# Kernel tuning notes

Measured on AMD Instinct MI355X. Metric: run time of the kernel, lower is better.

Reference implementation:

```python
import jax, jax.numpy as jnp
import numpy as np

N = 16384      # nodes per graph (128x128 image)
E = 9 * N      # 8-neighborhood + self edges
C = 512        # input feature channels
M = 32         # matrixSize


def _p(key, shape, scale=0.05):
    return jax.random.normal(key, shape, dtype=jnp.float32) * scale


def setup_inputs() -> dict:
    key = jax.random.key(0)
    ks = jax.random.split(key, 40)
    inp = {
        "cF": jax.random.normal(ks[0], (N, C), dtype=jnp.float32),
        "sF": jax.random.normal(ks[1], (N, C), dtype=jnp.float32),
        "content_edge_index": jax.random.randint(ks[2], (2, E), 0, N),
        "content_selections": jax.random.randint(ks[3], (E,), 0, 9),
        "style_edge_index": jax.random.randint(ks[4], (2, E), 0, N),
        "style_selections": jax.random.randint(ks[5], (E,), 0, 9),
        "compress_W": _p(ks[6], (1, C, M)),   # kernel_size=1 -> 1 selection
        "compress_b": _p(ks[7], (M,)),
        "unzip_W": _p(ks[8], (1, M, C)),
        "unzip_b": _p(ks[9], (C,)),
    }
    i = 10
    for net in ("cnet", "snet"):
        for j, (ci, co) in enumerate([(C, 256), (256, 128), (128, M)], 1):
            inp[f"{net}_W{j}"] = _p(ks[i], (9, ci, co)); i += 1  # kernel_size=3 -> 9 selections
            inp[f"{net}_b{j}"] = _p(ks[i], (co,)); i += 1
        inp[f"{net}_fcW"] = _p(ks[i], (M * M, M * M)); i += 1   # torch Linear [out,in]
        inp[f"{net}_fcb"] = _p(ks[i], (M * M,)); i += 1
    return inp


def sel_conv(x, edge_index, sel, W, b):
    """SelectionConv: per-selection weight, gather from src, scatter-add to dst.
    x: [N,Cin], W: [S,Cin,Cout]. Edges with selection >= S are masked (kernel_size=1)."""
    S = W.shape[0]
    t = jnp.einsum('nc,scd->snd', x, W)              # [S, N, Cout]
    src, dst = edge_index[0], edge_index[1]
    msgs = t[jnp.minimum(sel, S - 1), src]           # [E, Cout]
    msgs = jnp.where((sel < S)[:, None], msgs, 0.0)
    return jax.ops.segment_sum(msgs, dst, num_segments=x.shape[0]) + b


def cnn_net(x, ei, sel, W1, b1, W2, b2, W3, b3, fcW, fcb):
    h = jax.nn.relu(sel_conv(x, ei, sel, W1, b1))
    h = jax.nn.relu(sel_conv(h, ei, sel, W2, b2))
    h = sel_conv(h, ei, sel, W3, b3)                 # [N, M]
    g = (h.T @ h) / h.shape[0]                       # [M, M] gram
    return g.reshape(-1) @ fcW.T + fcb               # [M*M]


def reference(cF, sF, content_edge_index, content_selections, style_edge_index,
              style_selections, compress_W, compress_b, unzip_W, unzip_b,
              cnet_W1, cnet_b1, cnet_W2, cnet_b2, cnet_W3, cnet_b3, cnet_fcW, cnet_fcb,
              snet_W1, snet_b1, snet_W2, snet_b2, snet_W3, snet_b3, snet_fcW, snet_fcb):
    cMean = jnp.mean(cF, axis=0, keepdims=True)
    cFc = cF - cMean
    sMean = jnp.mean(sF, axis=0, keepdims=True)
    sFc = sF - sMean
    compress_content = sel_conv(cFc, content_edge_index, content_selections,
                                compress_W, compress_b)          # [N, M]
    m = compress_W.shape[2]
    cMat = cnn_net(cFc, content_edge_index, content_selections,
                   cnet_W1, cnet_b1, cnet_W2, cnet_b2, cnet_W3, cnet_b3,
                   cnet_fcW, cnet_fcb).reshape(m, m)
    sMat = cnn_net(sFc, style_edge_index, style_selections,
                   snet_W1, snet_b1, snet_W2, snet_b2, snet_W3, snet_b3,
                   snet_fcW, snet_fcb).reshape(m, m)
    transmatrix = sMat @ cMat                                    # [M, M]
    transfeature = (transmatrix @ compress_content.T).T          # [N, M]
    out = sel_conv(transfeature, content_edge_index, content_selections,
                   unzip_W, unzip_b) + sMean                     # [N, 512]
    return (out, transmatrix)
```

## Files before the change

kernel.cpp:

```cpp
#include <hip/hip_runtime.h>
#include <hip/hip_bf16.h>
#include <cstddef>
#include <cstdint>

#define NN 16384
#define EE (9*NN)
#define CC 512

typedef __attribute__((ext_vector_type(4))) float f32x4;
typedef __attribute__((ext_vector_type(8))) short bf16x8;

static inline int idiv(int a, int b){ return (a+b-1)/b; }

__device__ __forceinline__ float bf2f(unsigned short u){
    union{unsigned u; float f;} v; v.u = ((unsigned)u) << 16; return v.f;
}
__device__ __forceinline__ unsigned short f2bf(float f){
    union{float f; unsigned u;} v; v.f = f;
    unsigned r = v.u + 0x7fffu + ((v.u >> 16) & 1u);
    return (unsigned short)(r >> 16);
}

__device__ __forceinline__ void gload16(const void* gsrc, void* ldst){
    __builtin_amdgcn_global_load_lds(
        (const __attribute__((address_space(1))) unsigned int*)gsrc,
        (__attribute__((address_space(3))) unsigned int*)ldst,
        16, 0, 0);
}


__global__ void zero_i(int* __restrict__ p, int n){
    int i = blockIdx.x*256 + threadIdx.x; if (i < n) p[i] = 0;
}

__global__ void colsum2(const float* __restrict__ F0, float* __restrict__ cs0,
                        const float* __restrict__ F1, float* __restrict__ cs1){
    const float* F = blockIdx.z ? F1 : F0;
    float* cs = blockIdx.z ? cs1 : cs0;
    const int RPB = NN/256;
    int r0 = blockIdx.x * RPB;
    int c4 = threadIdx.x;
    float4 s = {0.f,0.f,0.f,0.f};
    for (int r = 0; r < RPB; ++r){
        float4 v = ((const float4*)(F + (size_t)(r0+r)*CC))[c4];
        s.x += v.x; s.y += v.y; s.z += v.z; s.w += v.w;
    }
    atomicAdd(&cs[c4*4+0], s.x);
    atomicAdd(&cs[c4*4+1], s.y);
    atomicAdd(&cs[c4*4+2], s.z);
    atomicAdd(&cs[c4*4+3], s.w);
}

__global__ void center2(const float* __restrict__ F0, const float* __restrict__ cs0,
                        ushort4* __restrict__ o0,
                        const float* __restrict__ F1, const float* __restrict__ cs1,
                        ushort4* __restrict__ o1){
    const float* F = blockIdx.z ? F1 : F0;
    const float* cs = blockIdx.z ? cs1 : cs0;
    ushort4* o = blockIdx.z ? o1 : o0;
    int i = blockIdx.x*256 + threadIdx.x;
    float4 v = ((const float4*)F)[i];
    int c = (i << 2) & (CC-1);
    float4 m = *(const float4*)(cs + c);
    ushort4 r;
    r.x = f2bf(v.x - m.x*(1.f/NN));
    r.y = f2bf(v.y - m.y*(1.f/NN));
    r.z = f2bf(v.z - m.z*(1.f/NN));
    r.w = f2bf(v.w - m.w*(1.f/NN));
    o[i] = r;
}

__global__ void wtransz(const float* __restrict__ W0, unsigned short* __restrict__ Wt0,
                        const float* __restrict__ W1, unsigned short* __restrict__ Wt1,
                        int S, int K, int Cout, int Npad, int Kpad){
    const float* W = blockIdx.z ? W1 : W0;
    unsigned short* Wt = blockIdx.z ? Wt1 : Wt0;
    int idx = blockIdx.x*256 + threadIdx.x;
    if (idx >= Npad*Kpad) return;
    int colp = idx / Kpad, k = idx - colp*Kpad;
    int s = colp / Cout, j = colp - s*Cout;
    float v = 0.f;
    if (s < S && k < K) v = W[((size_t)s*K + k)*Cout + j];
    Wt[idx] = f2bf(v);
}

__global__ void wtrans2z(const float* __restrict__ W0, const float* __restrict__ W1,
                         unsigned short* __restrict__ Wt0, unsigned short* __restrict__ Wt1,
                         int K, int Cout){
    __shared__ float tile[32][129];
    int s = blockIdx.z % 9;
    const float* W = (blockIdx.z < 9) ? W0 : W1;
    unsigned short* Wt = (blockIdx.z < 9) ? Wt0 : Wt1;
    int jb = blockIdx.x*128, kb = blockIdx.y*32;
    const float* Ws = W + (size_t)s*K*Cout;
    for (int r = 0; r < 32; ++r)
        tile[r][threadIdx.x] = Ws[(size_t)(kb+r)*Cout + jb + threadIdx.x];
    __syncthreads();
    int kk = threadIdx.x & 31, j0 = threadIdx.x >> 5;
    for (int jj = j0; jj < 128; jj += 4)
        Wt[(size_t)(s*Cout + jb + jj)*K + kb + kk] = f2bf(tile[kk][jj]);
}

__global__ void csr_count3(const int* __restrict__ cDst, const int* __restrict__ sDst,
                           const int* __restrict__ cSel,
                           int* __restrict__ cCnt, int* __restrict__ sCnt, int* __restrict__ cCnt0){
    int e = blockIdx.x*256 + threadIdx.x;
    if (e >= EE) return;
    int z = blockIdx.z;
    if (z == 0)      atomicAdd(&cCnt[cDst[e]], 1);
    else if (z == 1) atomicAdd(&sCnt[sDst[e]], 1);
    else if (cSel[e] == 0) atomicAdd(&cCnt0[cDst[e]], 1);
}
__global__ void csr_scan3(const int* __restrict__ c0, const int* __restrict__ c1,
                          const int* __restrict__ c2,
                          int* __restrict__ r0, int* __restrict__ r1, int* __restrict__ r2){
    const int* cnt = blockIdx.z==0 ? c0 : (blockIdx.z==1 ? c1 : c2);
    int* rowptr    = blockIdx.z==0 ? r0 : (blockIdx.z==1 ? r1 : r2);
    __shared__ int part[1024];
    int t = threadIdx.x;
    int base = t*16, s = 0;
    int local[16];
    #pragma unroll
    for (int i = 0; i < 16; ++i){ local[i] = s; s += cnt[base+i]; }
    part[t] = s; __syncthreads();
    for (int off = 1; off < 1024; off <<= 1){
        int v = (t >= off) ? part[t-off] : 0;
        __syncthreads();
        part[t] += v;
        __syncthreads();
    }
    int pre = (t == 0) ? 0 : part[t-1];
    #pragma unroll
    for (int i = 0; i < 16; ++i) rowptr[base+i] = pre + local[i];
    if (t == 1023) rowptr[NN] = part[1023];
}
__global__ void csr_fill3(const int* __restrict__ cSrc, const int* __restrict__ cDst,
                          const int* __restrict__ cSel,
                          const int* __restrict__ sSrc, const int* __restrict__ sDst,
                          const int* __restrict__ sSel,
                          const int* __restrict__ cRow, const int* __restrict__ sRow,
                          const int* __restrict__ cRow0,
                          int* __restrict__ cCur, int* __restrict__ sCur, int* __restrict__ cCur0,
                          int* __restrict__ cEl, int* __restrict__ sEl, int* __restrict__ cEl0){
    int e = blockIdx.x*256 + threadIdx.x;
    if (e >= EE) return;
    int z = blockIdx.z;
    if (z == 0){
        int d = cDst[e];
        int p = atomicAdd(&cCur[d], 1);
        cEl[cRow[d] + p] = (cSrc[e] << 4) | cSel[e];
    } else if (z == 1){
        int d = sDst[e];
        int p = atomicAdd(&sCur[d], 1);
        sEl[sRow[d] + p] = (sSrc[e] << 4) | sSel[e];
    } else if (cSel[e] == 0){
        int d = cDst[e];
        int p = atomicAdd(&cCur0[d], 1);
        cEl0[cRow0[d] + p] = cSrc[e];
    }
}

template<typename OutT>
__global__ __launch_bounds__(256, 2)
void mfma_gemm(const unsigned short* __restrict__ A0, const unsigned short* __restrict__ Bt0,
               OutT* __restrict__ C0,
               const unsigned short* __restrict__ A1, const unsigned short* __restrict__ Bt1,
               OutT* __restrict__ C1, int K, int N){
    const unsigned short* A  = blockIdx.z ? A1 : A0;
    const unsigned short* Bt = blockIdx.z ? Bt1 : Bt0;
    OutT* C = blockIdx.z ? C1 : C0;
    __shared__ __align__(16) unsigned short As[128*64];
    __shared__ __align__(16) unsigned short Bs[128*64];
    const int tid  = threadIdx.x;
    const int wave = tid >> 6, lane = tid & 63;
    const int row0 = blockIdx.y << 7, col0 = blockIdx.x << 7;
    const int wm = wave >> 1, wn = wave & 1;
    const int fr = lane & 15, fq = lane >> 4;
    f32x4 acc[4][4] = {};
    for (int k0 = 0; k0 < K; k0 += 64){
        __syncthreads();
        #pragma unroll
        for (int i = 0; i < 4; ++i){
            int chb = (wave*4 + i) * 64;
            int ch  = chb + lane;
            int r   = ch >> 3, c8 = ch & 7;
            gload16((const char*)(A  + (size_t)(row0 + r)*K + k0) + c8*16, As + chb*8);
            gload16((const char*)(Bt + (size_t)(col0 + r)*K + k0) + c8*16, Bs + chb*8);
        }
        __syncthreads();
        #pragma unroll
        for (int ks = 0; ks < 2; ++ks){
            bf16x8 av[4], bv[4];
            #pragma unroll
            for (int m = 0; m < 4; ++m)
                av[m] = *(const bf16x8*)(As + ((wm<<6)+(m<<4)+fr)*64 + (ks<<5) + (fq<<3));
            #pragma unroll
            for (int n = 0; n < 4; ++n)
                bv[n] = *(const bf16x8*)(Bs + ((wn<<6)+(n<<4)+fr)*64 + (ks<<5) + (fq<<3));
            #pragma unroll
            for (int m = 0; m < 4; ++m)
                #pragma unroll
                for (int n = 0; n < 4; ++n)
                    acc[m][n] = __builtin_amdgcn_mfma_f32_16x16x32_bf16(bv[n], av[m], acc[m][n], 0, 0, 0);
        }
    }
    #pragma unroll
    for (int m = 0; m < 4; ++m){
        int row = row0 + (wm<<6) + (m<<4) + fr;
        OutT* crow = C + (size_t)row*N + col0 + (wn<<6) + (fq<<2);
        #pragma unroll
        for (int n = 0; n < 4; ++n){
            if constexpr (sizeof(OutT) == 2){
                unsigned lo = f2bf(acc[m][n][0]) | ((unsigned)f2bf(acc[m][n][1]) << 16);
                unsigned hi = f2bf(acc[m][n][2]) | ((unsigned)f2bf(acc[m][n][3]) << 16);
                uint2 pk; pk.x = lo; pk.y = hi;
                *(uint2*)((unsigned short*)crow + (n<<4)) = pk;
            } else {
                float4 pk; pk.x = acc[m][n][0]; pk.y = acc[m][n][1];
                pk.z = acc[m][n][2]; pk.w = acc[m][n][3];
                *(float4*)((float*)crow + (n<<4)) = pk;
            }
        }
    }
}

template<int MQ, int NQ>
__device__ __forceinline__ void mfmaq(f32x4 (&acc)[8][4], bf16x8 (&a)[4][2], bf16x8 (&b)[2][2]){
    #pragma unroll
    for (int m = 0; m < 4; ++m)
        #pragma unroll
        for (int n = 0; n < 2; ++n)
            #pragma unroll
            for (int ks = 0; ks < 2; ++ks)
                acc[MQ*4+m][NQ*2+n] = __builtin_amdgcn_mfma_f32_16x16x32_bf16(
                    b[n][ks], a[m][ks], acc[MQ*4+m][NQ*2+n], 0, 0, 0);
}

#define MIDBAR() do{ __builtin_amdgcn_s_barrier(); \
                     asm volatile("s_waitcnt lgkmcnt(0)" ::: "memory"); \
                     __builtin_amdgcn_sched_barrier(0); \
                     __builtin_amdgcn_s_setprio(1); }while(0)
#define ENDBAR() do{ __builtin_amdgcn_s_setprio(0); \
                     __builtin_amdgcn_s_barrier(); }while(0)

template<int NK>
__global__ __launch_bounds__(512, 1)
void gemm8p(const unsigned short* __restrict__ Ain0, const unsigned short* __restrict__ Btin0,
            unsigned short* __restrict__ Cout0,
            const unsigned short* __restrict__ Ain1, const unsigned short* __restrict__ Btin1,
            unsigned short* __restrict__ Cout1, int N){
    constexpr int LDK = NK*64;
    const unsigned short* A  = blockIdx.z ? Ain1 : Ain0;
    const unsigned short* Bt = blockIdx.z ? Btin1 : Btin0;
    unsigned short* C = blockIdx.z ? Cout1 : Cout0;
    __shared__ __align__(16) unsigned short lds[2][4][8192];
    const int tid = threadIdx.x, w = tid >> 6, l = tid & 63;
    const int nbx = gridDim.x;
    const int nwg = gridDim.x * gridDim.y;
    int blin = blockIdx.y * nbx + blockIdx.x;
    int sw = (blin & 7) * (nwg >> 3) + (blin >> 3);
    const int bx = sw % nbx, by = sw / nbx;
    const int row0 = by << 8, col0 = bx << 8;
    const int wm = w >> 2, wn = w & 3;
    const int fr = l & 15, fq = l >> 4;

    f32x4 acc[8][4] = {};
    bf16x8 a[4][2], b01[2][2], b23[2][2];

    const unsigned short* gA = A + (size_t)row0 * LDK;
    const unsigned short* gB = Bt + (size_t)col0 * LDK;

    auto STG = [&](const unsigned short* gbase, int t, int half, unsigned short* ldsHalf){
        #pragma unroll
        for (int s = 0; s < 2; ++s){
            int o = s*8192 + w*1024 + l*16;
            int q = o ^ ((o >> 3) & 0x70);
            int row = q >> 7;
            gload16((const char*)(gbase + (size_t)(half*128 + row)*LDK + t*64) + (q & 127),
                    ldsHalf + s*4096 + w*512);
        }
    };
    auto LDA = [&](const unsigned short* half, int rb, int ks){
        int lg = (rb*16 + fr)*128 + ks*64 + fq*16;
        int ph = lg ^ ((fr & 7) << 4);
        return *(const bf16x8*)((const char*)half + ph);
    };

    STG(gA, 0, 0, &lds[0][0][0]); STG(gA, 0, 1, &lds[0][1][0]);
    STG(gB, 0, 0, &lds[0][2][0]); STG(gB, 0, 1, &lds[0][3][0]);
    STG(gB, 1, 0, &lds[1][2][0]); STG(gB, 1, 1, &lds[1][3][0]);
    asm volatile("s_waitcnt vmcnt(4)" ::: "memory");
    __builtin_amdgcn_s_barrier();

    const unsigned short* myA[2] = { &lds[0][wm][0], &lds[1][wm][0] };
    const unsigned short* myB[2] = { &lds[0][2+(wn>>1)][0], &lds[1][2+(wn>>1)][0] };
    const int brb = (wn & 1) * 4;

    for (int i = 0; i < NK/2; ++i){
        const int t0 = 2*i, t1 = 2*i + 1;
        #pragma unroll
        for (int m = 0; m < 4; ++m){ a[m][0] = LDA(myA[0], m, 0); a[m][1] = LDA(myA[0], m, 1); }
        #pragma unroll
        for (int n = 0; n < 2; ++n){ b01[n][0] = LDA(myB[0], brb+n, 0); b01[n][1] = LDA(myB[0], brb+n, 1); }
        STG(gA, t1, 0, &lds[1][0][0]);
        MIDBAR(); mfmaq<0,0>(acc, a, b01); ENDBAR();
        #pragma unroll
        for (int n = 0; n < 2; ++n){ b23[n][0] = LDA(myB[0], brb+2+n, 0); b23[n][1] = LDA(myB[0], brb+2+n, 1); }
        STG(gA, t1, 1, &lds[1][1][0]);
        MIDBAR(); mfmaq<0,1>(acc, a, b23); ENDBAR();
        #pragma unroll
        for (int m = 0; m < 4; ++m){ a[m][0] = LDA(myA[0], 4+m, 0); a[m][1] = LDA(myA[0], 4+m, 1); }
        STG(gB, t0+2, 0, &lds[0][2][0]);
        MIDBAR(); mfmaq<1,0>(acc, a, b01); ENDBAR();
        STG(gB, t0+2, 1, &lds[0][3][0]);
        asm volatile("s_waitcnt vmcnt(4)" ::: "memory");
        MIDBAR(); mfmaq<1,1>(acc, a, b23); ENDBAR();
        #pragma unroll
        for (int m = 0; m < 4; ++m){ a[m][0] = LDA(myA[1], m, 0); a[m][1] = LDA(myA[1], m, 1); }
        #pragma unroll
        for (int n = 0; n < 2; ++n){ b01[n][0] = LDA(myB[1], brb+n, 0); b01[n][1] = LDA(myB[1], brb+n, 1); }
        STG(gA, t0+2, 0, &lds[0][0][0]);
        MIDBAR(); mfmaq<0,0>(acc, a, b01); ENDBAR();
        #pragma unroll
        for (int n = 0; n < 2; ++n){ b23[n][0] = LDA(myB[1], brb+2+n, 0); b23[n][1] = LDA(myB[1], brb+2+n, 1); }
        STG(gA, t0+2, 1, &lds[0][1][0]);
        MIDBAR(); mfmaq<0,1>(acc, a, b23); ENDBAR();
        #pragma unroll
        for (int m = 0; m < 4; ++m){ a[m][0] = LDA(myA[1], 4+m, 0); a[m][1] = LDA(myA[1], 4+m, 1); }
        STG(gB, t1+2, 0, &lds[1][2][0]);
        MIDBAR(); mfmaq<1,0>(acc, a, b01); ENDBAR();
        STG(gB, t1+2, 1, &lds[1][3][0]);
        asm volatile("s_waitcnt vmcnt(4)" ::: "memory");
        MIDBAR(); mfmaq<1,1>(acc, a, b23); ENDBAR();
    }
    asm volatile("s_waitcnt vmcnt(0)" ::: "memory");

    #pragma unroll
    for (int m = 0; m < 8; ++m){
        int row = row0 + wm*128 + m*16 + fr;
        unsigned short* crow = C + (size_t)row*N + col0 + wn*64 + fq*4;
        #pragma unroll
        for (int n = 0; n < 4; ++n){
            unsigned lo = f2bf(acc[m][n][0]) | ((unsigned)f2bf(acc[m][n][1]) << 16);
            unsigned hi = f2bf(acc[m][n][2]) | ((unsigned)f2bf(acc[m][n][3]) << 16);
            uint2 pk; pk.x = lo; pk.y = hi;
            *(uint2*)(crow + (n<<4)) = pk;
        }
    }
}

template<int NT, typename OutT>
__global__ __launch_bounds__(256, 3)
void gemm_db(const unsigned short* __restrict__ A0, const unsigned short* __restrict__ Bt0,
             OutT* __restrict__ C0,
             const unsigned short* __restrict__ A1, const unsigned short* __restrict__ Bt1,
             OutT* __restrict__ C1, int N){
    constexpr int LDK = NT*32;
    const unsigned short* A  = blockIdx.z ? A1 : A0;
    const unsigned short* Bt = blockIdx.z ? Bt1 : Bt0;
    OutT* C = blockIdx.z ? C1 : C0;
    __shared__ __align__(16) unsigned short lds[2][2][4096];
    const int tid = threadIdx.x, w = tid >> 6, l = tid & 63;
    const int wm = w >> 1, wn = w & 1;
    const int fr = l & 15, fq = l >> 4;
    const int nbx = gridDim.x;
    const int nwg = gridDim.x * gridDim.y;
    int blin = blockIdx.y * nbx + blockIdx.x;
    int sw = (blin & 7) * (nwg >> 3) + (blin >> 3);
    const int bx = sw % nbx, by = sw / nbx;
    const int row0 = by << 7, col0 = bx << 7;

    const unsigned short* gA = A + (size_t)row0 * LDK;
    const unsigned short* gB = Bt + (size_t)col0 * LDK;

    auto STG = [&](int buf, int t){
        #pragma unroll
        for (int mtx = 0; mtx < 2; ++mtx){
            const unsigned short* gb = mtx ? gB : gA;
            #pragma unroll
            for (int ld = 0; ld < 2; ++ld){
                int o = (ld*256 + tid) * 16;
                int row = o >> 6;
                int kb = (o & 63) ^ ((row & 3) << 4);
                gload16((const char*)(gb + (size_t)row*LDK + t*32) + kb,
                        (char*)&lds[buf][mtx][0] + o);
            }
        }
    };

    f32x4 acc[4][4] = {};
    STG(0, 0);
    __syncthreads();
    for (int t = 0; t < NT; ++t){
        int cur = t & 1;
        if (t + 1 < NT) STG(cur ^ 1, t + 1);
        bf16x8 av[4], bv[4];
        #pragma unroll
        for (int m = 0; m < 4; ++m){
            int r = wm*64 + m*16 + fr;
            int p = (r*64 + fq*16) ^ ((r & 3) << 4);
            av[m] = *(const bf16x8*)((const char*)&lds[cur][0][0] + p);
        }
        #pragma unroll
        for (int n = 0; n < 4; ++n){
            int r = wn*64 + n*16 + fr;
            int p = (r*64 + fq*16) ^ ((r & 3) << 4);
            bv[n] = *(const bf16x8*)((const char*)&lds[cur][1][0] + p);
        }
        #pragma unroll
        for (int m = 0; m < 4; ++m)
            #pragma unroll
            for (int n = 0; n < 4; ++n)
                acc[m][n] = __builtin_amdgcn_mfma_f32_16x16x32_bf16(bv[n], av[m], acc[m][n], 0, 0, 0);
        __syncthreads();
    }

    #pragma unroll
    for (int m = 0; m < 4; ++m){
        int row = row0 + wm*64 + m*16 + fr;
        OutT* crow = C + (size_t)row*N + col0 + (wn<<6) + (fq<<2);
        #pragma unroll
        for (int n = 0; n < 4; ++n){
            if constexpr (sizeof(OutT) == 2){
                unsigned lo = f2bf(acc[m][n][0]) | ((unsigned)f2bf(acc[m][n][1]) << 16);
                unsigned hi = f2bf(acc[m][n][2]) | ((unsigned)f2bf(acc[m][n][3]) << 16);
                uint2 pk; pk.x = lo; pk.y = hi;
                *(uint2*)((unsigned short*)crow + (n<<4)) = pk;
            } else {
                float4 pk; pk.x = acc[m][n][0]; pk.y = acc[m][n][1];
                pk.z = acc[m][n][2]; pk.w = acc[m][n][3];
                *(float4*)((float*)crow + (n<<4)) = pk;
            }
        }
    }
}

template<typename TO, bool RELU>
__global__ void gather8z(const int* __restrict__ rp0, const int* __restrict__ el0,
                         const unsigned short* __restrict__ t0, const float* __restrict__ b0,
                         TO* __restrict__ o0,
                         const int* __restrict__ rp1, const int* __restrict__ el1,
                         const unsigned short* __restrict__ t1, const float* __restrict__ b1,
                         TO* __restrict__ o1,
                         int tStride, int coutShift){
    const int* rowptr = blockIdx.z ? rp1 : rp0;
    const int* elist  = blockIdx.z ? el1 : el0;
    const unsigned short* t = blockIdx.z ? t1 : t0;
    const float* bias = blockIdx.z ? b1 : b0;
    TO* out = blockIdx.z ? o1 : o0;
    int idx = blockIdx.x*256 + threadIdx.x;
    int chSh = coutShift - 3;
    int d = idx >> chSh;
    int c0 = (idx & ((1 << chSh) - 1)) << 3;
    float acc[8];
    {
        const float4* bb = (const float4*)(bias + c0);
        float4 a = bb[0], b = bb[1];
        acc[0]=a.x; acc[1]=a.y; acc[2]=a.z; acc[3]=a.w;
        acc[4]=b.x; acc[5]=b.y; acc[6]=b.z; acc[7]=b.w;
    }
    int j1 = rowptr[d+1];
    #pragma unroll 2
    for (int j = rowptr[d]; j < j1; ++j){
        int p = elist[j];
        int s = p & 15, sr = p >> 4;
        bf16x8 v = *(const bf16x8*)(t + (size_t)sr*tStride + (s << coutShift) + c0);
        #pragma unroll
        for (int k = 0; k < 8; ++k) acc[k] += bf2f((unsigned short)v[k]);
    }
    if (RELU){
        #pragma unroll
        for (int k = 0; k < 8; ++k) acc[k] = fmaxf(acc[k], 0.f);
    }
    if constexpr (sizeof(TO) == 2){
        union { bf16x8 v; unsigned short u[8]; } r;
        #pragma unroll
        for (int k = 0; k < 8; ++k) r.u[k] = f2bf(acc[k]);
        *(bf16x8*)((unsigned short*)out + ((size_t)d << coutShift) + c0) = r.v;
    } else {
        float4 a = {acc[0],acc[1],acc[2],acc[3]};
        float4 b = {acc[4],acc[5],acc[6],acc[7]};
        float4* op = (float4*)((float*)out + ((size_t)d << coutShift) + c0);
        op[0] = a; op[1] = b;
    }
}

template<bool ADDV>
__global__ void gather4f(const int* __restrict__ rowptr, const int* __restrict__ elist,
                         const float* __restrict__ t,
                         const float* __restrict__ bias, const float* __restrict__ addvec,
                         float* __restrict__ out, int tStride, int coutShift){
    int idx = blockIdx.x*256 + threadIdx.x;
    int chSh = coutShift - 2;
    int d = idx >> chSh;
    int c0 = (idx & ((1 << chSh) - 1)) << 2;
    float4 bb = *(const float4*)(bias + c0);
    float acc0 = bb.x, acc1 = bb.y, acc2 = bb.z, acc3 = bb.w;
    if (ADDV){
        float4 av = *(const float4*)(addvec + c0);
        acc0 += av.x*(1.f/NN); acc1 += av.y*(1.f/NN);
        acc2 += av.z*(1.f/NN); acc3 += av.w*(1.f/NN);
    }
    int j1 = rowptr[d+1];
    #pragma unroll 2
    for (int j = rowptr[d]; j < j1; ++j){
        int sr = elist[j];
        float4 v = *(const float4*)(t + (size_t)sr*tStride + c0);
        acc0 += v.x; acc1 += v.y; acc2 += v.z; acc3 += v.w;
    }
    float4 r = {acc0, acc1, acc2, acc3};
    *(float4*)(out + ((size_t)d << coutShift) + c0) = r;
}

__global__ void gram2(const float* __restrict__ h0, float* __restrict__ g0,
                      const float* __restrict__ h1, float* __restrict__ g1){
    const float* h = blockIdx.z ? h1 : h0;
    float* g = blockIdx.z ? g1 : g0;
    const int RPB = NN/64;
    int r0 = blockIdx.x*RPB;
    int i = threadIdx.x >> 5, j = threadIdx.x & 31;
    float s = 0.f;
    for (int r = 0; r < RPB; ++r){
        const float* row = h + (size_t)(r0+r)*32;
        s += row[i]*row[j];
    }
    atomicAdd(&g[threadIdx.x], s);
}

__global__ void fc2(const float* __restrict__ g0, const float* __restrict__ fcW0,
                    const float* __restrict__ fcb0, float* __restrict__ o0,
                    const float* __restrict__ g1, const float* __restrict__ fcW1,
                    const float* __restrict__ fcb1, float* __restrict__ o1){
    const float* g   = blockIdx.z ? g1 : g0;
    const float* fcW = blockIdx.z ? fcW1 : fcW0;
    const float* fcb = blockIdx.z ? fcb1 : fcb0;
    float* outMat    = blockIdx.z ? o1 : o0;
    int i = blockIdx.x;
    float s = 0.f;
    for (int j = threadIdx.x; j < 1024; j += 256)
        s += g[j] * (1.f/NN) * fcW[(size_t)i*1024 + j];
    __shared__ float red[256];
    red[threadIdx.x] = s; __syncthreads();
    for (int off = 128; off > 0; off >>= 1){
        if (threadIdx.x < off) red[threadIdx.x] += red[threadIdx.x+off];
        __syncthreads();
    }
    if (threadIdx.x == 0) outMat[i] = red[0] + fcb[i];
}

__global__ void mm32_kernel(const float* __restrict__ A, const float* __restrict__ B,
                            float* __restrict__ T){
    int i = threadIdx.x >> 5, j = threadIdx.x & 31;
    float s = 0.f;
    for (int k = 0; k < 32; ++k) s += A[i*32+k]*B[k*32+j];
    T[threadIdx.x] = s;
}

__global__ void tf_cvt_kernel(const float* __restrict__ cc, const float* __restrict__ T,
                              unsigned short* __restrict__ tfbB){
    __shared__ float Ts[1024];
    for (int i = threadIdx.x; i < 1024; i += blockDim.x) Ts[i] = T[i];
    __syncthreads();
    int idx = blockIdx.x*blockDim.x + threadIdx.x;
    int n = idx >> 5, i = idx & 31;
    float s = 0.f;
    const float* crow = cc + (size_t)n*32;
    #pragma unroll
    for (int j = 0; j < 32; ++j) s += crow[j] * Ts[i*32+j];
    tfbB[(size_t)n*64 + i] = f2bf(s);
    tfbB[(size_t)n*64 + 32 + i] = 0;
}

extern "C" void kernel_launch(void* const* d_in, const int* in_sizes, int n_in,
                              void* d_out, int out_size, void* d_ws, size_t ws_size,
                              hipStream_t stream){
    const float* cF   = (const float*)d_in[0];
    const float* sF   = (const float*)d_in[1];
    const int*   cEI  = (const int*)d_in[2];
    const int*   cSel = (const int*)d_in[3];
    const int*   sEI  = (const int*)d_in[4];
    const int*   sSel = (const int*)d_in[5];
    const float* compW= (const float*)d_in[6];
    const float* compB= (const float*)d_in[7];
    const float* unzW = (const float*)d_in[8];
    const float* unzB = (const float*)d_in[9];
    const float* cW1=(const float*)d_in[10]; const float* cB1=(const float*)d_in[11];
    const float* cW2=(const float*)d_in[12]; const float* cB2=(const float*)d_in[13];
    const float* cW3=(const float*)d_in[14]; const float* cB3=(const float*)d_in[15];
    const float* cFW=(const float*)d_in[16]; const float* cFB=(const float*)d_in[17];
    const float* sW1=(const float*)d_in[18]; const float* sB1=(const float*)d_in[19];
    const float* sW2=(const float*)d_in[20]; const float* sB2=(const float*)d_in[21];
    const float* sW3=(const float*)d_in[22]; const float* sB3=(const float*)d_in[23];
    const float* sFW=(const float*)d_in[24]; const float* sFB=(const float*)d_in[25];

    float* out  = (float*)d_out;
    float* Tmat = out + (size_t)NN*CC;

    char* w = (char*)d_ws;
    auto alloc = [&](size_t b)->char*{ char* p = w; w += (b + 255) & ~(size_t)255; return p; };
    float* cCol = (float*)alloc(512*4);
    float* sCol = (float*)alloc(512*4);
    float* cg   = (float*)alloc(1024*4);
    float* sg   = (float*)alloc(1024*4);
    float* cMat = (float*)alloc(1024*4);
    float* sMat = (float*)alloc(1024*4);
    int* cCnt = (int*)alloc(NN*4);
    int* cCur = (int*)alloc(NN*4);
    int* sCnt = (int*)alloc(NN*4);
    int* sCur = (int*)alloc(NN*4);
    int* cCnt0= (int*)alloc(NN*4);
    int* cCur0= (int*)alloc(NN*4);
    int* cRow = (int*)alloc((NN+1)*4);
    int* sRow = (int*)alloc((NN+1)*4);
    int* cRow0= (int*)alloc((NN+1)*4);
    int* cEl  = (int*)alloc(EE*4);
    int* sEl  = (int*)alloc(EE*4);
    int* cEl0 = (int*)alloc(EE*4);
    float* ccbuf = (float*)alloc((size_t)NN*32*4);
    unsigned short* tfbB = (unsigned short*)alloc((size_t)NN*64*2);
    unsigned short* wtC1 = (unsigned short*)alloc((size_t)2304*512*2);
    unsigned short* wtC2 = (unsigned short*)alloc((size_t)1280*256*2);
    unsigned short* wtC3 = (unsigned short*)alloc((size_t)384*128*2);
    unsigned short* wtS1 = (unsigned short*)alloc((size_t)2304*512*2);
    unsigned short* wtS2 = (unsigned short*)alloc((size_t)1280*256*2);
    unsigned short* wtS3 = (unsigned short*)alloc((size_t)384*128*2);
    unsigned short* wtCo = (unsigned short*)alloc((size_t)128*512*2);
    unsigned short* wtU  = (unsigned short*)alloc((size_t)512*64*2);
    unsigned short* cFcB = (unsigned short*)alloc((size_t)NN*512*2);
    unsigned short* sFcB = (unsigned short*)alloc((size_t)NN*512*2);
    float* h3c = (float*)alloc((size_t)NN*32*4);
    float* h3s = (float*)alloc((size_t)NN*32*4);
    unsigned short* tC = (unsigned short*)alloc((size_t)NN*2304*2);
    unsigned short* tS = (unsigned short*)alloc((size_t)NN*2304*2);
    float* tFc = (float*)tC;
    unsigned short* h1c = cFcB;
    unsigned short* h1s = sFcB;
    unsigned short* h2c = cFcB + (size_t)NN*256;
    unsigned short* h2s = sFcB + (size_t)NN*256;

    const int* cSrc = cEI; const int* cDst = cEI + EE;
    const int* sSrc = sEI; const int* sDst = sEI + EE;

    int zeroInts = (int)(((char*)cCur0 - (char*)d_ws)/4) + NN;
    zero_i<<<idiv(zeroInts,256),256,0,stream>>>((int*)d_ws, zeroInts);

    colsum2<<<dim3(256,1,2),128,0,stream>>>(cF, cCol, sF, sCol);
    center2<<<dim3(NN*CC/1024,1,2),256,0,stream>>>(cF, cCol, (ushort4*)cFcB,
                                                   sF, sCol, (ushort4*)sFcB);

    wtrans2z<<<dim3(2,16,18),128,0,stream>>>(cW1, sW1, wtC1, wtS1, 512, 256);
    wtrans2z<<<dim3(1,8,18),128,0,stream>>>(cW2, sW2, wtC2, wtS2, 256, 128);
    wtransz<<<dim3(idiv(384*128,256),1,2),256,0,stream>>>(cW3, wtC3, sW3, wtS3, 9,128,32, 384,128);
    wtransz<<<dim3(idiv(128*512,256),1,1),256,0,stream>>>(compW, wtCo, compW, wtCo, 1,512,32, 128,512);
    wtransz<<<dim3(idiv(512*64,256),1,1),256,0,stream>>>(unzW, wtU, unzW, wtU, 1,32,512, 512,64);

    csr_count3<<<dim3(idiv(EE,256),1,3),256,0,stream>>>(cDst, sDst, cSel, cCnt, sCnt, cCnt0);
    csr_scan3<<<dim3(1,1,3),1024,0,stream>>>(cCnt, sCnt, cCnt0, cRow, sRow, cRow0);
    csr_fill3<<<dim3(idiv(EE,256),1,3),256,0,stream>>>(cSrc,cDst,cSel, sSrc,sDst,sSel,
                                                       cRow,sRow,cRow0, cCur,sCur,cCur0,
                                                       cEl,sEl,cEl0);

    mfma_gemm<float><<<dim3(1,128,1),256,0,stream>>>(cFcB, wtCo, tFc,
                                                     cFcB, wtCo, tFc, 512, 128);
    gather4f<false><<<NN*8/256,256,0,stream>>>(cRow0,cEl0,tFc,compB,nullptr,ccbuf,128,5);

    gemm_db<16,unsigned short><<<dim3(18,128,2),256,0,stream>>>(cFcB, wtC1, tC,
                                                                sFcB, wtS1, tS, 2304);
    gather8z<unsigned short,true><<<dim3(2048,1,2),256,0,stream>>>(
        cRow,cEl,tC,cB1,h1c, sRow,sEl,tS,sB1,h1s, 2304, 8);
    gemm8p<4><<<dim3(5,64,2),512,0,stream>>>(h1c, wtC2, tC, h1s, wtS2, tS, 1280);
    gather8z<unsigned short,true><<<dim3(1024,1,2),256,0,stream>>>(
        cRow,cEl,tC,cB2,h2c, sRow,sEl,tS,sB2,h2s, 1280, 7);
    mfma_gemm<unsigned short><<<dim3(3,128,2),256,0,stream>>>(h2c, wtC3, tC,
                                                              h2s, wtS3, tS, 128, 384);
    gather8z<float,false><<<dim3(256,1,2),256,0,stream>>>(
        cRow,cEl,tC,cB3,h3c, sRow,sEl,tS,sB3,h3s, 384, 5);
    gram2<<<dim3(64,1,2),1024,0,stream>>>(h3c, cg, h3s, sg);
    fc2<<<dim3(1024,1,2),256,0,stream>>>(cg,cFW,cFB,cMat, sg,sFW,sFB,sMat);

    mm32_kernel<<<1,1024,0,stream>>>(sMat, cMat, Tmat);
    tf_cvt_kernel<<<NN*32/256,256,0,stream>>>(ccbuf, Tmat, tfbB);

    mfma_gemm<float><<<dim3(4,128,1),256,0,stream>>>(tfbB, wtU, tFc,
                                                     tfbB, wtU, tFc, 64, 512);
    gather4f<true><<<NN*128/256,256,0,stream>>>(cRow0,cEl0,tFc,unzB,sCol,out,512,9);
}
```

Before: 420.6 us.

## Replace 256x256 ping-pong GEMM with double-buffered 128-tile GEMM and new LDS swizzle

Removes the 8-wave 256x256 gemm8p kernel used for the second conv layer and routes that GEMM through the existing gemm_db double-buffered kernel with a 10x128x2 grid. The gemm_db occupancy hint rises from 3 to 4 blocks per CU. Its LDS XOR swizzle now uses bits of (row>>1) instead of (row&3) to cut bank conflicts on the 64-byte rows. The smaller tile gives more blocks and better occupancy for this short-K GEMM (K=256). In exchange it reloads operands more often and drops the hand-scheduled prefetch pipeline.

```diff
diff --git a/kernel.cpp b/kernel.cpp
--- a/kernel.cpp
+++ b/kernel.cpp
@@ -224,133 +224,8 @@
     }
 }
 
-template<int MQ, int NQ>
-__device__ __forceinline__ void mfmaq(f32x4 (&acc)[8][4], bf16x8 (&a)[4][2], bf16x8 (&b)[2][2]){
-    #pragma unroll
-    for (int m = 0; m < 4; ++m)
-        #pragma unroll
-        for (int n = 0; n < 2; ++n)
-            #pragma unroll
-            for (int ks = 0; ks < 2; ++ks)
-                acc[MQ*4+m][NQ*2+n] = __builtin_amdgcn_mfma_f32_16x16x32_bf16(
-                    b[n][ks], a[m][ks], acc[MQ*4+m][NQ*2+n], 0, 0, 0);
-}
-
-#define MIDBAR() do{ __builtin_amdgcn_s_barrier(); \
-                     asm volatile("s_waitcnt lgkmcnt(0)" ::: "memory"); \
-                     __builtin_amdgcn_sched_barrier(0); \
-                     __builtin_amdgcn_s_setprio(1); }while(0)
-#define ENDBAR() do{ __builtin_amdgcn_s_setprio(0); \
-                     __builtin_amdgcn_s_barrier(); }while(0)
-
-template<int NK>
-__global__ __launch_bounds__(512, 1)
-void gemm8p(const unsigned short* __restrict__ Ain0, const unsigned short* __restrict__ Btin0,
-            unsigned short* __restrict__ Cout0,
-            const unsigned short* __restrict__ Ain1, const unsigned short* __restrict__ Btin1,
-            unsigned short* __restrict__ Cout1, int N){
-    constexpr int LDK = NK*64;
-    const unsigned short* A  = blockIdx.z ? Ain1 : Ain0;
-    const unsigned short* Bt = blockIdx.z ? Btin1 : Btin0;
-    unsigned short* C = blockIdx.z ? Cout1 : Cout0;
-    __shared__ __align__(16) unsigned short lds[2][4][8192];
-    const int tid = threadIdx.x, w = tid >> 6, l = tid & 63;
-    const int nbx = gridDim.x;
-    const int nwg = gridDim.x * gridDim.y;
-    int blin = blockIdx.y * nbx + blockIdx.x;
-    int sw = (blin & 7) * (nwg >> 3) + (blin >> 3);
-    const int bx = sw % nbx, by = sw / nbx;
-    const int row0 = by << 8, col0 = bx << 8;
-    const int wm = w >> 2, wn = w & 3;
-    const int fr = l & 15, fq = l >> 4;
-
-    f32x4 acc[8][4] = {};
-    bf16x8 a[4][2], b01[2][2], b23[2][2];
-
-    const unsigned short* gA = A + (size_t)row0 * LDK;
-    const unsigned short* gB = Bt + (size_t)col0 * LDK;
-
-    auto STG = [&](const unsigned short* gbase, int t, int half, unsigned short* ldsHalf){
-        #pragma unroll
-        for (int s = 0; s < 2; ++s){
-            int o = s*8192 + w*1024 + l*16;
-            int q = o ^ ((o >> 3) & 0x70);
-            int row = q >> 7;
-            gload16((const char*)(gbase + (size_t)(half*128 + row)*LDK + t*64) + (q & 127),
-                    ldsHalf + s*4096 + w*512);
-        }
-    };
-    auto LDA = [&](const unsigned short* half, int rb, int ks){
-        int lg = (rb*16 + fr)*128 + ks*64 + fq*16;
-        int ph = lg ^ ((fr & 7) << 4);
-        return *(const bf16x8*)((const char*)half + ph);
-    };
-
-    STG(gA, 0, 0, &lds[0][0][0]); STG(gA, 0, 1, &lds[0][1][0]);
-    STG(gB, 0, 0, &lds[0][2][0]); STG(gB, 0, 1, &lds[0][3][0]);
-    STG(gB, 1, 0, &lds[1][2][0]); STG(gB, 1, 1, &lds[1][3][0]);
-    asm volatile("s_waitcnt vmcnt(4)" ::: "memory");
-    __builtin_amdgcn_s_barrier();
-
-    const unsigned short* myA[2] = { &lds[0][wm][0], &lds[1][wm][0] };
-    const unsigned short* myB[2] = { &lds[0][2+(wn>>1)][0], &lds[1][2+(wn>>1)][0] };
-    const int brb = (wn & 1) * 4;
-
-    for (int i = 0; i < NK/2; ++i){
-        const int t0 = 2*i, t1 = 2*i + 1;
-        #pragma unroll
-        for (int m = 0; m < 4; ++m){ a[m][0] = LDA(myA[0], m, 0); a[m][1] = LDA(myA[0], m, 1); }
-        #pragma unroll
-        for (int n = 0; n < 2; ++n){ b01[n][0] = LDA(myB[0], brb+n, 0); b01[n][1] = LDA(myB[0], brb+n, 1); }
-        STG(gA, t1, 0, &lds[1][0][0]);
-        MIDBAR(); mfmaq<0,0>(acc, a, b01); ENDBAR();
-        #pragma unroll
-        for (int n = 0; n < 2; ++n){ b23[n][0] = LDA(myB[0], brb+2+n, 0); b23[n][1] = LDA(myB[0], brb+2+n, 1); }
-        STG(gA, t1, 1, &lds[1][1][0]);
-        MIDBAR(); mfmaq<0,1>(acc, a, b23); ENDBAR();
-        #pragma unroll
-        for (int m = 0; m < 4; ++m){ a[m][0] = LDA(myA[0], 4+m, 0); a[m][1] = LDA(myA[0], 4+m, 1); }
-        STG(gB, t0+2, 0, &lds[0][2][0]);
-        MIDBAR(); mfmaq<1,0>(acc, a, b01); ENDBAR();
-        STG(gB, t0+2, 1, &lds[0][3][0]);
-        asm volatile("s_waitcnt vmcnt(4)" ::: "memory");
-        MIDBAR(); mfmaq<1,1>(acc, a, b23); ENDBAR();
-        #pragma unroll
-        for (int m = 0; m < 4; ++m){ a[m][0] = LDA(myA[1], m, 0); a[m][1] = LDA(myA[1], m, 1); }
-        #pragma unroll
-        for (int n = 0; n < 2; ++n){ b01[n][0] = LDA(myB[1], brb+n, 0); b01[n][1] = LDA(myB[1], brb+n, 1); }
-        STG(gA, t0+2, 0, &lds[0][0][0]);
-        MIDBAR(); mfmaq<0,0>(acc, a, b01); ENDBAR();
-        #pragma unroll
-        for (int n = 0; n < 2; ++n){ b23[n][0] = LDA(myB[1], brb+2+n, 0); b23[n][1] = LDA(myB[1], brb+2+n, 1); }
-        STG(gA, t0+2, 1, &lds[0][1][0]);
-        MIDBAR(); mfmaq<0,1>(acc, a, b23); ENDBAR();
-        #pragma unroll
-        for (int m = 0; m < 4; ++m){ a[m][0] = LDA(myA[1], 4+m, 0); a[m][1] = LDA(myA[1], 4+m, 1); }
-        STG(gB, t1+2, 0, &lds[1][2][0]);
-        MIDBAR(); mfmaq<1,0>(acc, a, b01); ENDBAR();
-        STG(gB, t1+2, 1, &lds[1][3][0]);
-        asm volatile("s_waitcnt vmcnt(4)" ::: "memory");
-        MIDBAR(); mfmaq<1,1>(acc, a, b23); ENDBAR();
-    }
-    asm volatile("s_waitcnt vmcnt(0)" ::: "memory");
-
-    #pragma unroll
-    for (int m = 0; m < 8; ++m){
-        int row = row0 + wm*128 + m*16 + fr;
-        unsigned short* crow = C + (size_t)row*N + col0 + wn*64 + fq*4;
-        #pragma unroll
-        for (int n = 0; n < 4; ++n){
-            unsigned lo = f2bf(acc[m][n][0]) | ((unsigned)f2bf(acc[m][n][1]) << 16);
-            unsigned hi = f2bf(acc[m][n][2]) | ((unsigned)f2bf(acc[m][n][3]) << 16);
-            uint2 pk; pk.x = lo; pk.y = hi;
-            *(uint2*)(crow + (n<<4)) = pk;
-        }
-    }
-}
-
 template<int NT, typename OutT>
-__global__ __launch_bounds__(256, 3)
+__global__ __launch_bounds__(256, 4)
 void gemm_db(const unsigned short* __restrict__ A0, const unsigned short* __restrict__ Bt0,
              OutT* __restrict__ C0,
              const unsigned short* __restrict__ A1, const unsigned short* __restrict__ Bt1,
@@ -381,7 +256,7 @@
             for (int ld = 0; ld < 2; ++ld){
                 int o = (ld*256 + tid) * 16;
                 int row = o >> 6;
-                int kb = (o & 63) ^ ((row & 3) << 4);
+                int kb = (o & 63) ^ (((o >> 7) & 3) << 4);
                 gload16((const char*)(gb + (size_t)row*LDK + t*32) + kb,
                         (char*)&lds[buf][mtx][0] + o);
             }
@@ -398,13 +273,13 @@
         #pragma unroll
         for (int m = 0; m < 4; ++m){
             int r = wm*64 + m*16 + fr;
-            int p = (r*64 + fq*16) ^ ((r & 3) << 4);
+            int p = (r*64 + fq*16) ^ (((r >> 1) & 3) << 4);
             av[m] = *(const bf16x8*)((const char*)&lds[cur][0][0] + p);
         }
         #pragma unroll
         for (int n = 0; n < 4; ++n){
             int r = wn*64 + n*16 + fr;
-            int p = (r*64 + fq*16) ^ ((r & 3) << 4);
+            int p = (r*64 + fq*16) ^ (((r >> 1) & 3) << 4);
             bv[n] = *(const bf16x8*)((const char*)&lds[cur][1][0] + p);
         }
         #pragma unroll
@@ -668,7 +543,8 @@
                                                                 sFcB, wtS1, tS, 2304);
     gather8z<unsigned short,true><<<dim3(2048,1,2),256,0,stream>>>(
         cRow,cEl,tC,cB1,h1c, sRow,sEl,tS,sB1,h1s, 2304, 8);
-    gemm8p<4><<<dim3(5,64,2),512,0,stream>>>(h1c, wtC2, tC, h1s, wtS2, tS, 1280);
+    gemm_db<8,unsigned short><<<dim3(10,128,2),256,0,stream>>>(h1c, wtC2, tC,
+                                                               h1s, wtS2, tS, 1280);
     gather8z<unsigned short,true><<<dim3(1024,1,2),256,0,stream>>>(
         cRow,cEl,tC,cB2,h2c, sRow,sEl,tS,sB2,h2s, 1280, 7);
     mfma_gemm<unsigned short><<<dim3(3,128,2),256,0,stream>>>(h2c, wtC3, tC,
```

After: 407.9 us. -3.0%, faster.
